# Performance work log

Measured on AMD Instinct MI355X. Metric: run time of the kernel, lower is better.

## Reference

```python
import jax, jax.numpy as jnp
import numpy as np

B, LX, LY, D = 8, 2048, 2048, 256

def setup_inputs() -> dict:
    key = jax.random.key(0)
    k1, k2, k3, k4 = jax.random.split(key, 4)
    x = jax.random.normal(k1, (B, LX, D), dtype=jnp.float32)
    y = jax.random.normal(k2, (B, LY, D), dtype=jnp.float32)
    y_mask = jax.random.randint(k3, (B, LY), 0, 2).astype(jnp.bool_)
    W = jax.random.normal(k4, (D, D), dtype=jnp.float32) * (1.0 / np.sqrt(D))
    b = jnp.zeros((D,), dtype=jnp.float32)
    return {"x": x, "y": y, "y_mask": y_mask, "W": W, "b": b}

def reference(x, y, y_mask, W, b):
    # shared linear + relu projection (torch Linear: x @ W.T + b)
    x_proj = jax.nn.relu(jnp.einsum('bld,ed->ble', x, W) + b)  # [B,LX,D]
    y_proj = jax.nn.relu(jnp.einsum('bld,ed->ble', y, W) + b)  # [B,LY,D]
    scores = jnp.einsum('bxd,byd->bxy', x_proj, y_proj)        # [B,LX,LY]
    scores = jnp.where(y_mask[:, None, :], -jnp.inf, scores)
    alpha = jax.nn.softmax(scores, axis=-1)                    # [B,LX,LY]
    return jnp.einsum('bxy,byd->bxd', alpha, y)                # [B,LX,D]
```

## Files before the change

### kernel.cpp

```cpp
#include <hip/hip_runtime.h>

typedef __attribute__((ext_vector_type(8))) short short8;
typedef _Float16 half8 __attribute__((ext_vector_type(8)));
typedef __attribute__((ext_vector_type(4))) float f32x4;
typedef __attribute__((ext_vector_type(4))) unsigned int uint4v;
typedef __attribute__((ext_vector_type(2))) unsigned int uint2v;

#define B_   8
#define LX_  2048
#define LY_  2048
#define D_   256
#define NROW (B_ * LX_)

__device__ __forceinline__ unsigned short f2bf(float f) {
  unsigned u = __builtin_bit_cast(unsigned, f);
  u += 0x7FFF + ((u >> 16) & 1);
  return (unsigned short)(u >> 16);
}
__device__ __forceinline__ float bf2f(unsigned short h) {
  unsigned u = ((unsigned)h) << 16;
  return __builtin_bit_cast(float, u);
}

__global__ __launch_bounds__(256) void prep_kernel(
    const float* __restrict__ W, unsigned short* __restrict__ Whi,
    unsigned short* __restrict__ Wlo,
    const int* __restrict__ MASK, int* __restrict__ CIDX, int* __restrict__ Lc) {
  int t = threadIdx.x;
  if (blockIdx.x >= 8) {
    int base = (blockIdx.x - 8) * 2048 + t * 8;
    f32x4 f0 = *(const f32x4*)(W + base);
    f32x4 f1 = *(const f32x4*)(W + base + 4);
    float v[8] = {f0[0], f0[1], f0[2], f0[3], f1[0], f1[1], f1[2], f1[3]};
    unsigned short h[8], l[8];
    for (int j = 0; j < 8; ++j) {
      h[j] = f2bf(v[j]);
      l[j] = f2bf(v[j] - bf2f(h[j]));
    }
    uint4v vh = {(unsigned)h[0] | ((unsigned)h[1] << 16), (unsigned)h[2] | ((unsigned)h[3] << 16),
                 (unsigned)h[4] | ((unsigned)h[5] << 16), (unsigned)h[6] | ((unsigned)h[7] << 16)};
    uint4v vl = {(unsigned)l[0] | ((unsigned)l[1] << 16), (unsigned)l[2] | ((unsigned)l[3] << 16),
                 (unsigned)l[4] | ((unsigned)l[5] << 16), (unsigned)l[6] | ((unsigned)l[7] << 16)};
    *(uint4v*)(Whi + base) = vh;
    *(uint4v*)(Wlo + base) = vl;
    return;
  }
  __shared__ int s[256];
  int b = blockIdx.x;
  int f[8];
  int cnt = 0;
  for (int k = 0; k < 8; ++k) {
    f[k] = (MASK[b * 2048 + t * 8 + k] == 0) ? 1 : 0;
    cnt += f[k];
  }
  s[t] = cnt;
  __syncthreads();
  for (int off = 1; off < 256; off <<= 1) {
    int v = (t >= off) ? s[t - off] : 0;
    __syncthreads();
    s[t] += v;
    __syncthreads();
  }
  if (t == 255) Lc[b] = s[255];
  int off = s[t] - cnt;
  for (int k = 0; k < 8; ++k) {
    int j = t * 8 + k;
    if (f[k]) CIDX[b * 2048 + (off++)] = j;
  }
}

__global__ __launch_bounds__(256, 2) void projgather_kernel(
    const float* __restrict__ X, const float* __restrict__ Y,
    const float* __restrict__ bias,
    const unsigned short* __restrict__ Whi, const unsigned short* __restrict__ Wlo,
    const int* __restrict__ CIDX, const int* __restrict__ Lc,
    _Float16* __restrict__ XP, _Float16* __restrict__ YPc,
    _Float16* __restrict__ YTc) {
  __shared__ __align__(16) unsigned char smem[51200];
  int t = threadIdx.x;

  if (blockIdx.x >= 512) {
    _Float16 (*tile)[72] = (_Float16(*)[72])smem;
    int id = blockIdx.x - 512;
    int db = id & 3, nb = (id >> 2) & 31, b = id >> 7;
    int lc = Lc[b];
    int end = (lc + 31) & ~31;
    if (nb * 64 >= end) return;
    int nl = t >> 2, ds = t & 3;
    int j = nb * 64 + nl;
    int idx = (j < lc) ? CIDX[b * 2048 + j] : 0;
    const float* src = Y + (size_t)(b * LY_ + idx) * D_ + db * 64 + ds * 16;
    for (int i = 0; i < 4; ++i) {
      f32x4 f = *(const f32x4*)(src + i * 4);
      for (int k = 0; k < 4; ++k) tile[ds * 16 + i * 4 + k][nl] = (_Float16)f[k];
    }
    __syncthreads();
    int dl = t >> 2, nsub = t & 3;
    uint4v v0 = *(const uint4v*)&tile[dl][nsub * 16];
    uint4v v1 = *(const uint4v*)&tile[dl][nsub * 16 + 8];
    _Float16* dst = YTc + (size_t)(b * D_ + db * 64 + dl) * LY_ + nb * 64 + nsub * 16;
    *(uint4v*)(dst) = v0;
    *(uint4v*)(dst + 8) = v1;
    return;
  }

  unsigned short (*Ah)[40] = (unsigned short(*)[40])(smem);
  unsigned short (*Al)[40] = (unsigned short(*)[40])(smem + 5120);
  unsigned short (*Bh)[40] = (unsigned short(*)[40])(smem + 10240);
  unsigned short (*Bl)[40] = (unsigned short(*)[40])(smem + 30720);

  int lane = t & 63, wave = t >> 6;
  int q = lane >> 4, n15 = lane & 15;
  int arow = t >> 2, aseg = t & 3;
  int erow = t >> 2, ec = t & 3;

  bool isX = blockIdx.x < 256;
  int m0 = 0, b = 0, slot0 = 0, lcb = 0;
  const float* arow_ptr;
  if (isX) {
    m0 = blockIdx.x * 64;
    arow_ptr = X + (size_t)(m0 + arow) * D_;
  } else {
    int id = blockIdx.x - 256;
    b = id >> 5;
    int rb = id & 31;
    lcb = Lc[b];
    slot0 = rb * 64;
    if (slot0 >= lcb) return;
    int sl = slot0 + arow;
    int grow = (sl < lcb) ? CIDX[b * 2048 + sl] : 0;
    arow_ptr = Y + (size_t)(b * 2048 + grow) * D_;
  }

  f32x4 acc[4][4];
  for (int mt = 0; mt < 4; ++mt)
    for (int nt = 0; nt < 4; ++nt) acc[mt][nt] = (f32x4){0.f, 0.f, 0.f, 0.f};

  f32x4 pa[2];
  uint4v pbh[4], pbl[4];
#define PROJ_PF(kc)                                                            \
  {                                                                            \
    for (int i = 0; i < 2; ++i)                                                \
      pa[i] = *(const f32x4*)(arow_ptr + (kc) * 32 + (aseg + i * 4) * 4);      \
    for (int p = 0; p < 4; ++p) {                                              \
      int e = p * 64 + erow;                                                   \
      pbh[p] = *(const uint4v*)(Whi + (size_t)e * D_ + (kc) * 32 + ec * 8);    \
      pbl[p] = *(const uint4v*)(Wlo + (size_t)e * D_ + (kc) * 32 + ec * 8);    \
    }                                                                          \
  }

  PROJ_PF(0);

  for (int kc = 0; kc < 8; ++kc) {
    __syncthreads();
    for (int i = 0; i < 2; ++i) {
      int seg = aseg + i * 4;
      f32x4 f = pa[i];
      unsigned short h[4], l[4];
      for (int j = 0; j < 4; ++j) {
        h[j] = f2bf(f[j]);
        l[j] = f2bf(f[j] - bf2f(h[j]));
      }
      uint2v vh = {(unsigned)h[0] | ((unsigned)h[1] << 16),
                   (unsigned)h[2] | ((unsigned)h[3] << 16)};
      uint2v vl = {(unsigned)l[0] | ((unsigned)l[1] << 16),
                   (unsigned)l[2] | ((unsigned)l[3] << 16)};
      *(uint2v*)&Ah[arow][seg * 4] = vh;
      *(uint2v*)&Al[arow][seg * 4] = vl;
    }
    for (int p = 0; p < 4; ++p) {
      int e = p * 64 + erow;
      *(uint4v*)&Bh[e][ec * 8] = pbh[p];
      *(uint4v*)&Bl[e][ec * 8] = pbl[p];
    }
    if (kc < 7) PROJ_PF(kc + 1);
    __syncthreads();

    short8 afh[4], afl[4], bfh[4], bfl[4];
    for (int mt = 0; mt < 4; ++mt) {
      afh[mt] = *(const short8*)&Ah[mt * 16 + n15][q * 8];
      afl[mt] = *(const short8*)&Al[mt * 16 + n15][q * 8];
    }
    for (int nt = 0; nt < 4; ++nt) {
      bfh[nt] = *(const short8*)&Bh[wave * 64 + nt * 16 + n15][q * 8];
      bfl[nt] = *(const short8*)&Bl[wave * 64 + nt * 16 + n15][q * 8];
    }
    for (int mt = 0; mt < 4; ++mt)
      for (int nt = 0; nt < 4; ++nt) {
        acc[mt][nt] = __builtin_amdgcn_mfma_f32_16x16x32_bf16(afh[mt], bfh[nt], acc[mt][nt], 0, 0, 0);
        acc[mt][nt] = __builtin_amdgcn_mfma_f32_16x16x32_bf16(afl[mt], bfh[nt], acc[mt][nt], 0, 0, 0);
        acc[mt][nt] = __builtin_amdgcn_mfma_f32_16x16x32_bf16(afh[mt], bfl[nt], acc[mt][nt], 0, 0, 0);
      }
  }
#undef PROJ_PF

  __syncthreads();
  _Float16 (*epi)[264] = (_Float16(*)[264])smem;
  for (int nt = 0; nt < 4; ++nt) {
    int e = wave * 64 + nt * 16 + n15;
    float bv = bias[e];
    for (int mt = 0; mt < 4; ++mt)
      for (int r = 0; r < 4; ++r) {
        float v = acc[mt][nt][r] + bv;
        v = v > 0.f ? v : 0.f;
        epi[mt * 16 + q * 4 + r][e] = (_Float16)v;
      }
  }
  __syncthreads();
  int row = t >> 2, seg = t & 3;
  bool valid = isX || (slot0 + row < lcb);
  if (valid) {
    _Float16* drp = isX ? (XP + (size_t)(m0 + row) * D_)
                        : (YPc + (size_t)(b * 2048 + slot0 + row) * D_);
    for (int k = 0; k < 8; ++k) {
      uint4v v = *(const uint4v*)&epi[row][seg * 64 + k * 8];
      *(uint4v*)(drp + seg * 64 + k * 8) = v;
    }
  }
}

__global__ __launch_bounds__(256, 2) void flash_kernel(
    const _Float16* __restrict__ XP, const _Float16* __restrict__ YPc,
    const _Float16* __restrict__ YTc, const int* __restrict__ Lc,
    _Float16* __restrict__ PO, float* __restrict__ Pm, float* __restrict__ Pl,
    int lg) {
  __shared__ __align__(16) _Float16 yp_t[32][264];
  __shared__ __align__(16) _Float16 yT_t[256][32];
  __shared__ __align__(16) _Float16 pbuf[4][16][40];

  int t = threadIdx.x;
  int lane = t & 63, wave = t >> 6;
  int q = lane >> 4, n15 = lane & 15;
  int ns = 1 << lg;
  int half = blockIdx.x & (ns - 1);
  int xb = (blockIdx.x >> lg) & 31;
  int b = blockIdx.x >> (lg + 5);
  int row0 = xb * 64 + wave * 16;

  int lc = Lc[b];
  int T  = (lc + 31) >> 5;
  int tstart = (T * half) >> lg;
  int tend   = (T * (half + 1)) >> lg;

  half8 a[8];
  const _Float16* xrow = XP + (size_t)(b * LX_ + row0 + n15) * D_ + q * 8;
  for (int kk = 0; kk < 8; ++kk) a[kk] = *(const half8*)(xrow + kk * 32);

  half8 lones;
  for (int j = 0; j < 8; ++j) lones[j] = (n15 == 0) ? (_Float16)1 : (_Float16)0;

  float m_r[4];
  for (int r = 0; r < 4; ++r) m_r[r] = -1e30f;
  f32x4 lacc = {0.f, 0.f, 0.f, 0.f};
  f32x4 oacc[16];
  for (int dt = 0; dt < 16; ++dt) oacc[dt] = (f32x4){0.f, 0.f, 0.f, 0.f};

  const _Float16* ypb = YPc + (size_t)b * LY_ * D_;
  const _Float16* yTb = YTc + (size_t)b * D_ * LY_;

  uint4v pr[8];
#define PREFETCH(tt)                                                          \
  {                                                                           \
    int y0p = (tt) * 32;                                                      \
    for (int i = 0; i < 4; ++i) {                                             \
      int c = t + i * 256;                                                    \
      pr[i] = *(const uint4v*)(ypb + (size_t)(y0p + (c >> 5)) * D_ + (c & 31) * 8); \
    }                                                                         \
    for (int i = 0; i < 4; ++i) {                                             \
      int c = t + i * 256;                                                    \
      pr[4 + i] = *(const uint4v*)(yTb + (size_t)(c >> 2) * LY_ + y0p + (c & 3) * 8); \
    }                                                                         \
  }

  if (tstart < tend) PREFETCH(tstart);

  for (int tt = tstart; tt < tend; ++tt) {
    int y0 = tt * 32;
    __syncthreads();
    for (int i = 0; i < 4; ++i) {
      int c = t + i * 256;
      *(uint4v*)&yp_t[c >> 5][(c & 31) * 8] = pr[i];
    }
    for (int i = 0; i < 4; ++i) {
      int c = t + i * 256;
      int rT = c >> 2, pc = (c & 3) ^ (rT & 3);
      *(uint4v*)&yT_t[rT][pc * 8] = pr[4 + i];
    }
    if (tt + 1 < tend) PREFETCH(tt + 1);
    __syncthreads();

    f32x4 S0 = {0.f, 0.f, 0.f, 0.f}, S1 = {0.f, 0.f, 0.f, 0.f};
    for (int kk = 0; kk < 8; ++kk) {
      half8 b0 = *(const half8*)&yp_t[n15][kk * 32 + q * 8];
      S0 = __builtin_amdgcn_mfma_f32_16x16x32_f16(a[kk], b0, S0, 0, 0, 0);
    }
    for (int kk = 0; kk < 8; ++kk) {
      half8 b1 = *(const half8*)&yp_t[16 + n15][kk * 32 + q * 8];
      S1 = __builtin_amdgcn_mfma_f32_16x16x32_f16(a[kk], b1, S1, 0, 0, 0);
    }
    bool mk0 = (y0 + n15) >= lc;
    bool mk1 = (y0 + 16 + n15) >= lc;

    float al[4];
    _Float16 ph0[4], ph1[4];
    bool need = false;
    for (int r = 0; r < 4; ++r) {
      float s0 = mk0 ? -1e30f : S0[r];
      float s1 = mk1 ? -1e30f : S1[r];
      float tm = fmaxf(s0, s1);
      tm = fmaxf(tm, __shfl_xor(tm, 1));
      tm = fmaxf(tm, __shfl_xor(tm, 2));
      tm = fmaxf(tm, __shfl_xor(tm, 4));
      tm = fmaxf(tm, __shfl_xor(tm, 8));
      float mn = fmaxf(m_r[r], tm);
      al[r] = __expf(m_r[r] - mn);
      m_r[r] = mn;
      ph0[r] = (_Float16)__expf(s0 - mn);
      ph1[r] = (_Float16)__expf(s1 - mn);
      need = need || (al[r] != 1.0f);
    }
    if (__ballot(need)) {
      for (int dt = 0; dt < 16; ++dt)
        for (int r = 0; r < 4; ++r) oacc[dt][r] *= al[r];
      for (int r = 0; r < 4; ++r) lacc[r] *= al[r];
    }
    for (int r = 0; r < 4; ++r) {
      pbuf[wave][q * 4 + r][n15] = ph0[r];
      pbuf[wave][q * 4 + r][16 + n15] = ph1[r];
    }
    half8 pa = *(const half8*)&pbuf[wave][n15][q * 8];
    lacc = __builtin_amdgcn_mfma_f32_16x16x32_f16(pa, lones, lacc, 0, 0, 0);
    for (int dt = 0; dt < 16; ++dt) {
      int rT = dt * 16 + n15;
      half8 bb = *(const half8*)&yT_t[rT][(q ^ (rT & 3)) * 8];
      oacc[dt] = __builtin_amdgcn_mfma_f32_16x16x32_f16(pa, bb, oacc[dt], 0, 0, 0);
    }
  }
#undef PREFETCH

  size_t prow = (size_t)(half * B_ + b) * LX_ + row0;
  _Float16* po = PO + prow * D_;
  for (int dt = 0; dt < 16; ++dt)
    for (int r = 0; r < 4; ++r)
      po[(size_t)(q * 4 + r) * D_ + dt * 16 + n15] = (_Float16)oacc[dt][r];
  if (n15 == 0) {
    for (int r = 0; r < 4; ++r) {
      Pm[prow + q * 4 + r] = m_r[r];
      Pl[prow + q * 4 + r] = lacc[r];
    }
  }
}

__global__ __launch_bounds__(256) void merge_kernel(
    const _Float16* __restrict__ PO, const float* __restrict__ Pm,
    const float* __restrict__ Pl, float* __restrict__ OUT, int ns) {
  int c = blockIdx.x * 256 + threadIdx.x;
  int row = c >> 5, seg = c & 31;
  float m = Pm[row];
  for (int p = 1; p < ns; ++p) m = fmaxf(m, Pm[p * NROW + row]);
  float denom = 0.f;
  f32x4 o0 = {0.f, 0.f, 0.f, 0.f}, o1 = {0.f, 0.f, 0.f, 0.f};
  for (int p = 0; p < ns; ++p) {
    float w = __expf(Pm[p * NROW + row] - m);
    denom += Pl[p * NROW + row] * w;
    const _Float16* pp = PO + ((size_t)p * NROW + row) * D_ + seg * 8;
    half8 a = *(const half8*)pp;
    for (int j = 0; j < 4; ++j) o0[j] += (float)a[j] * w;
    for (int j = 0; j < 4; ++j) o1[j] += (float)a[4 + j] * w;
  }
  float inv = 1.0f / denom;
  for (int j = 0; j < 4; ++j) o0[j] *= inv;
  for (int j = 0; j < 4; ++j) o1[j] *= inv;
  float* o = OUT + (size_t)row * D_ + seg * 8;
  *(f32x4*)o = o0;
  *(f32x4*)(o + 4) = o1;
}

extern "C" void kernel_launch(void* const* d_in, const int* in_sizes, int n_in,
                              void* d_out, int out_size, void* d_ws, size_t ws_size,
                              hipStream_t stream) {
  const float* x     = (const float*)d_in[0];
  const float* y     = (const float*)d_in[1];
  const int*   ymask = (const int*)  d_in[2];
  const float* W     = (const float*)d_in[3];
  const float* bias  = (const float*)d_in[4];
  float* out = (float*)d_out;

  size_t need4 = 262144ull
               + 3ull * 8388608ull
               + 4ull * 8388608ull
               + 2ull * 262144ull
               + 65536ull + 4096ull;
  int lg = (ws_size >= need4) ? 2 : 1;
  int nsplit = 1 << lg;

  char* ws = (char*)d_ws;
  size_t o = 0;
  unsigned short* Whi = (unsigned short*)(ws + o); o += 131072;
  unsigned short* Wlo = (unsigned short*)(ws + o); o += 131072;
  _Float16* XP  = (_Float16*)(ws + o); o += 8388608;
  _Float16* YPc = (_Float16*)(ws + o); o += 8388608;
  _Float16* YTc = (_Float16*)(ws + o); o += 8388608;
  _Float16* PO  = (_Float16*)(ws + o); o += (size_t)nsplit * 8388608;
  float* Pm   = (float*)(ws + o); o += (size_t)nsplit * 65536;
  float* Pl   = (float*)(ws + o); o += (size_t)nsplit * 65536;
  int*   CIDX = (int*)  (ws + o); o += 65536;
  int*   Lc   = (int*)  (ws + o);

  prep_kernel<<<40, 256, 0, stream>>>(W, Whi, Wlo, ymask, CIDX, Lc);
  projgather_kernel<<<1536, 256, 0, stream>>>(x, y, bias, Whi, Wlo, CIDX, Lc,
                                              XP, YPc, YTc);
  flash_kernel<<<256 * nsplit, 256, 0, stream>>>(XP, YPc, YTc, Lc, PO, Pm, Pl, lg);
  merge_kernel<<<2048, 256, 0, stream>>>(PO, Pm, Pl, out, nsplit);
}
```

Baseline: 161.7 us.

## Split key range three ways, drop register prefetch, raise flash occupancy to 3

Changes the flash kernel's key-range split from a power of two (2 or 4) to 3 or 2, selected by workspace size, using division instead of shifts. It removes the register double-buffered prefetch of the next Y tile and loads directly before the barrier, then raises launch bounds to 3 blocks per SM so that occupancy hides latency instead. The intent is fewer registers, more resident waves and a better-balanced grid (768 blocks). The cost is exposed global-load latency per tile and possible register spilling under the tighter bound.

```diff
diff --git a/kernel.cpp b/kernel.cpp
--- a/kernel.cpp
+++ b/kernel.cpp
@@ -219,11 +219,11 @@
   }
 }
 
-__global__ __launch_bounds__(256, 2) void flash_kernel(
+__global__ __launch_bounds__(256, 3) void flash_kernel(
     const _Float16* __restrict__ XP, const _Float16* __restrict__ YPc,
     const _Float16* __restrict__ YTc, const int* __restrict__ Lc,
     _Float16* __restrict__ PO, float* __restrict__ Pm, float* __restrict__ Pl,
-    int lg) {
+    int ns) {
   __shared__ __align__(16) _Float16 yp_t[32][264];
   __shared__ __align__(16) _Float16 yT_t[256][32];
   __shared__ __align__(16) _Float16 pbuf[4][16][40];
@@ -231,16 +231,16 @@
   int t = threadIdx.x;
   int lane = t & 63, wave = t >> 6;
   int q = lane >> 4, n15 = lane & 15;
-  int ns = 1 << lg;
-  int half = blockIdx.x & (ns - 1);
-  int xb = (blockIdx.x >> lg) & 31;
-  int b = blockIdx.x >> (lg + 5);
+  int p = blockIdx.x % ns;
+  int rest = blockIdx.x / ns;
+  int xb = rest & 31;
+  int b = rest >> 5;
   int row0 = xb * 64 + wave * 16;
 
   int lc = Lc[b];
   int T  = (lc + 31) >> 5;
-  int tstart = (T * half) >> lg;
-  int tend   = (T * (half + 1)) >> lg;
+  int tstart = (T * p) / ns;
+  int tend   = (T * (p + 1)) / ns;
 
   half8 a[8];
   const _Float16* xrow = XP + (size_t)(b * LX_ + row0 + n15) * D_ + q * 8;
@@ -258,35 +258,27 @@
   const _Float16* ypb = YPc + (size_t)b * LY_ * D_;
   const _Float16* yTb = YTc + (size_t)b * D_ * LY_;
 
-  uint4v pr[8];
-#define PREFETCH(tt)                                                          \
-  {                                                                           \
-    int y0p = (tt) * 32;                                                      \
-    for (int i = 0; i < 4; ++i) {                                             \
-      int c = t + i * 256;                                                    \
-      pr[i] = *(const uint4v*)(ypb + (size_t)(y0p + (c >> 5)) * D_ + (c & 31) * 8); \
-    }                                                                         \
-    for (int i = 0; i < 4; ++i) {                                             \
-      int c = t + i * 256;                                                    \
-      pr[4 + i] = *(const uint4v*)(yTb + (size_t)(c >> 2) * LY_ + y0p + (c & 3) * 8); \
-    }                                                                         \
-  }
-
-  if (tstart < tend) PREFETCH(tstart);
-
   for (int tt = tstart; tt < tend; ++tt) {
     int y0 = tt * 32;
-    __syncthreads();
+    uint4v ld[8];
     for (int i = 0; i < 4; ++i) {
       int c = t + i * 256;
-      *(uint4v*)&yp_t[c >> 5][(c & 31) * 8] = pr[i];
+      ld[i] = *(const uint4v*)(ypb + (size_t)(y0 + (c >> 5)) * D_ + (c & 31) * 8);
+    }
+    for (int i = 0; i < 4; ++i) {
+      int c = t + i * 256;
+      ld[4 + i] = *(const uint4v*)(yTb + (size_t)(c >> 2) * LY_ + y0 + (c & 3) * 8);
+    }
+    __syncthreads();
+    for (int i = 0; i < 4; ++i) {
+      int c = t + i * 256;
+      *(uint4v*)&yp_t[c >> 5][(c & 31) * 8] = ld[i];
     }
     for (int i = 0; i < 4; ++i) {
       int c = t + i * 256;
       int rT = c >> 2, pc = (c & 3) ^ (rT & 3);
-      *(uint4v*)&yT_t[rT][pc * 8] = pr[4 + i];
-    }
-    if (tt + 1 < tend) PREFETCH(tt + 1);
+      *(uint4v*)&yT_t[rT][pc * 8] = ld[4 + i];
+    }
     __syncthreads();
 
     f32x4 S0 = {0.f, 0.f, 0.f, 0.f}, S1 = {0.f, 0.f, 0.f, 0.f};
@@ -336,9 +328,8 @@
       oacc[dt] = __builtin_amdgcn_mfma_f32_16x16x32_f16(pa, bb, oacc[dt], 0, 0, 0);
     }
   }
-#undef PREFETCH
-
-  size_t prow = (size_t)(half * B_ + b) * LX_ + row0;
+
+  size_t prow = (size_t)(p * B_ + b) * LX_ + row0;
   _Float16* po = PO + prow * D_;
   for (int dt = 0; dt < 16; ++dt)
     for (int r = 0; r < 4; ++r)
@@ -386,13 +377,12 @@
   const float* bias  = (const float*)d_in[4];
   float* out = (float*)d_out;
 
-  size_t need4 = 262144ull
+  size_t need3 = 262144ull
                + 3ull * 8388608ull
-               + 4ull * 8388608ull
-               + 2ull * 262144ull
+               + 3ull * 8388608ull
+               + 6ull * 65536ull
                + 65536ull + 4096ull;
-  int lg = (ws_size >= need4) ? 2 : 1;
-  int nsplit = 1 << lg;
+  int ns = (ws_size >= need3) ? 3 : 2;
 
   char* ws = (char*)d_ws;
   size_t o = 0;
@@ -401,15 +391,15 @@
   _Float16* XP  = (_Float16*)(ws + o); o += 8388608;
   _Float16* YPc = (_Float16*)(ws + o); o += 8388608;
   _Float16* YTc = (_Float16*)(ws + o); o += 8388608;
-  _Float16* PO  = (_Float16*)(ws + o); o += (size_t)nsplit * 8388608;
-  float* Pm   = (float*)(ws + o); o += (size_t)nsplit * 65536;
-  float* Pl   = (float*)(ws + o); o += (size_t)nsplit * 65536;
+  _Float16* PO  = (_Float16*)(ws + o); o += (size_t)ns * 8388608;
+  float* Pm   = (float*)(ws + o); o += (size_t)ns * 65536;
+  float* Pl   = (float*)(ws + o); o += (size_t)ns * 65536;
   int*   CIDX = (int*)  (ws + o); o += 65536;
   int*   Lc   = (int*)  (ws + o);
 
   prep_kernel<<<40, 256, 0, stream>>>(W, Whi, Wlo, ymask, CIDX, Lc);
   projgather_kernel<<<1536, 256, 0, stream>>>(x, y, bias, Whi, Wlo, CIDX, Lc,
                                               XP, YPc, YTc);
-  flash_kernel<<<256 * nsplit, 256, 0, stream>>>(XP, YPc, YTc, Lc, PO, Pm, Pl, lg);
-  merge_kernel<<<2048, 256, 0, stream>>>(PO, Pm, Pl, out, nsplit);
-}
+  flash_kernel<<<256 * ns, 256, 0, stream>>>(XP, YPc, YTc, Lc, PO, Pm, Pl, ns);
+  merge_kernel<<<2048, 256, 0, stream>>>(PO, Pm, Pl, out, ns);
+}
```

Measured after the change: 160.7 us. No clear change (-0.6%).
